# Optimization experiments

Measured on AMD Instinct MI355X. Metric: run time of the kernel, lower is better.

## Reference

```python
import jax, jax.numpy as jnp
import numpy as np

EPS = 1e-12          # matches torch F.normalize eps
NOW = 3600.0         # fixed 'current time'; timestamps are in [0,1)
TIME_DECAY = 3600.0  # temporal decay constant from the module

def setup_inputs() -> dict:
    key = jax.random.key(0)
    k1, k2, k3, k4, k5 = jax.random.split(key, 5)
    M, D, S = 100000, 768, 2
    return {
        "query_features": jax.random.normal(k1, (D,), dtype=jnp.float32),
        "location": jax.random.normal(k2, (S,), dtype=jnp.float32),
        "memory_features": jax.random.normal(k3, (M, D), dtype=jnp.float32),
        "memory_locations": jax.random.normal(k4, (M, S), dtype=jnp.float32),
        "memory_metadata": jax.random.uniform(k5, (M, 4), dtype=jnp.float32),
        "k": 5,
    }

def reference(query_features, location, memory_features, memory_locations, memory_metadata, k):
    # --- cosine similarity: normalize query and memory rows (F.normalize semantics) ---
    q_norm = query_features / jnp.maximum(jnp.linalg.norm(query_features), EPS)      # [D]
    m_norms = jnp.maximum(jnp.linalg.norm(memory_features, axis=1, keepdims=True), EPS)
    m_norm = memory_features / m_norms                                               # [M, D]
    sim_scores = m_norm @ q_norm                                                     # [M] GEMV

    # --- spatial score: 1 / (1 + euclidean distance to query location) ---
    dists = jnp.linalg.norm(memory_locations - location[None, :], axis=1)            # [M]
    spatial_scores = 1.0 / (1.0 + dists)

    # --- temporal score: exp(-age / 3600) ---
    strengths = memory_metadata[:, 0]
    timestamps = memory_metadata[:, 1]
    ages = NOW - timestamps
    temporal_scores = jnp.exp(-ages / TIME_DECAY)

    combined = (0.5 * sim_scores + 0.3 * spatial_scores + 0.2 * temporal_scores) * strengths

    top_scores, top_indices = jax.lax.top_k(combined, k)
    return top_scores, top_indices
```

## Files before the change

kernel.cpp:

```cpp
#include <hip/hip_runtime.h>
#include <math.h>

#define EPS   1e-12f
#define NOW_T 3600.0f
#define TDEC  3600.0f
#define K     5
#define D     768

__global__ __launch_bounds__(256) void score_kernel(
    const float* __restrict__ q,
    const float* __restrict__ loc,
    const float* __restrict__ feat,
    const float* __restrict__ mloc,
    const float* __restrict__ meta,
    float* __restrict__ scores,
    int M)
{
    const int tid = threadIdx.x;
    const int c   = tid & 15;
    const int g   = tid >> 4;
    const int row = blockIdx.x * 16 + g;

    const float* qp = q + c * 4;
    float4 qv[12];
    float qss = 0.f;
    #pragma unroll
    for (int j = 0; j < 12; ++j) {
        qv[j] = *(const float4*)(qp + j * 64);
        qss = fmaf(qv[j].x, qv[j].x, qss);
        qss = fmaf(qv[j].y, qv[j].y, qss);
        qss = fmaf(qv[j].z, qv[j].z, qss);
        qss = fmaf(qv[j].w, qv[j].w, qss);
    }
    #pragma unroll
    for (int m = 1; m < 16; m <<= 1) qss += __shfl_xor(qss, m);
    const float inv_qn = 1.0f / fmaxf(sqrtf(qss), EPS);

    float dot = 0.f, ss = 0.f;
    if (row < M) {
        const float* r = feat + (size_t)row * D + c * 4;
        #pragma unroll
        for (int j = 0; j < 12; ++j) {
            float4 f = *(const float4*)(r + j * 64);
            dot = fmaf(f.x, qv[j].x, dot); ss = fmaf(f.x, f.x, ss);
            dot = fmaf(f.y, qv[j].y, dot); ss = fmaf(f.y, f.y, ss);
            dot = fmaf(f.z, qv[j].z, dot); ss = fmaf(f.z, f.z, ss);
            dot = fmaf(f.w, qv[j].w, dot); ss = fmaf(f.w, f.w, ss);
        }
    }
    #pragma unroll
    for (int m = 1; m < 16; m <<= 1) {
        dot += __shfl_xor(dot, m);
        ss  += __shfl_xor(ss,  m);
    }

    if (row < M && c == 0) {
        float sim = dot * inv_qn / fmaxf(sqrtf(ss), EPS);
        float2 ml = *(const float2*)(mloc + (size_t)row * 2);
        float4 md = *(const float4*)(meta + (size_t)row * 4);
        float dx = ml.x - loc[0], dy = ml.y - loc[1];
        float dist = sqrtf(dx * dx + dy * dy);
        float spatial  = 1.0f / (1.0f + dist);
        float temporal = expf((md.y - NOW_T) / TDEC);
        scores[row] = (0.5f * sim + 0.3f * spatial + 0.2f * temporal) * md.x;
    }
}

__device__ __forceinline__ void consider(float (&v)[K], int (&ix)[K], float s, int i)
{
    if (s > v[K - 1]) {
        int j = K - 1;
        #pragma unroll
        for (int t = K - 1; t > 0; --t) {
            if (v[t - 1] < s) { v[t] = v[t - 1]; ix[t] = ix[t - 1]; j = t - 1; }
        }
        v[j] = s; ix[j] = i;
    }
}

__global__ __launch_bounds__(1024) void topk_kernel(
    const float* __restrict__ scores, int M, float* __restrict__ out)
{
    __shared__ float s_val[1024 * K];
    __shared__ int   s_idx[1024 * K];

    const int tid = threadIdx.x;
    float v[K]; int ix[K];
    #pragma unroll
    for (int j = 0; j < K; ++j) { v[j] = -INFINITY; ix[j] = -1; }

    const int M4 = M >> 2;
    const float4* s4 = (const float4*)scores;
    for (int i = tid; i < M4; i += 1024) {
        float4 s = s4[i];
        consider(v, ix, s.x, 4 * i + 0);
        consider(v, ix, s.y, 4 * i + 1);
        consider(v, ix, s.z, 4 * i + 2);
        consider(v, ix, s.w, 4 * i + 3);
    }
    for (int i = (M4 << 2) + tid; i < M; i += 1024)
        consider(v, ix, scores[i], i);

    #pragma unroll
    for (int j = 0; j < K; ++j) { s_val[tid * K + j] = v[j]; s_idx[tid * K + j] = ix[j]; }
    __syncthreads();

    for (int sz = 1024 >> 1; sz >= 1; sz >>= 1) {
        if (tid < sz) {
            const float* pv = &s_val[(tid + sz) * K];
            const int*   pi = &s_idx[(tid + sz) * K];
            float mv[K]; int mi[K];
            int a = 0, b = 0;
            #pragma unroll
            for (int j = 0; j < K; ++j) {
                bool takeA = (b >= K) || (a < K && v[a] >= pv[b]);
                if (takeA) { mv[j] = v[a];  mi[j] = ix[a]; ++a; }
                else       { mv[j] = pv[b]; mi[j] = pi[b]; ++b; }
            }
            #pragma unroll
            for (int j = 0; j < K; ++j) {
                v[j] = mv[j]; ix[j] = mi[j];
                s_val[tid * K + j] = v[j]; s_idx[tid * K + j] = ix[j];
            }
        }
        __syncthreads();
    }

    if (tid == 0) {
        #pragma unroll
        for (int j = 0; j < K; ++j) {
            out[j]     = v[j];
            out[K + j] = (float)ix[j];
        }
    }
}

extern "C" void kernel_launch(void* const* d_in, const int* in_sizes, int n_in,
                              void* d_out, int out_size, void* d_ws, size_t ws_size,
                              hipStream_t stream) {
    const float* q    = (const float*)d_in[0];
    const float* loc  = (const float*)d_in[1];
    const float* feat = (const float*)d_in[2];
    const float* mloc = (const float*)d_in[3];
    const float* meta = (const float*)d_in[4];
    const int M = in_sizes[2] / D;

    float* scores = (float*)d_ws;

    score_kernel<<<(M + 15) / 16, 256, 0, stream>>>(q, loc, feat, mloc, meta, scores, M);
    topk_kernel<<<1, 1024, 0, stream>>>(scores, M, (float*)d_out);
}
```

Baseline: 448.5 us.

## Fuse scoring with per-block top-k and merge small candidate set

The scoring kernel becomes a persistent grid-stride kernel with a fixed grid of 2048 blocks. Each 16-lane group keeps a running top-5 and the block reduces these to 5 candidates written to the workspace. The single-block top-k kernel now merges only about 10K candidates instead of scanning all 100K scores, which removes the serial full-array pass and the score write and read. In exchange, each block does a serial top-k merge in thread 0, and the fixed grid size may change how the feature-matrix stream is spread across CUs.

```diff
diff --git a/kernel.cpp b/kernel.cpp
--- a/kernel.cpp
+++ b/kernel.cpp
@@ -6,20 +6,33 @@
 #define TDEC  3600.0f
 #define K     5
 #define D     768
+#define GRID  2048
 
-__global__ __launch_bounds__(256) void score_kernel(
+__device__ __forceinline__ void consider(float (&v)[K], int (&ix)[K], float s, int i)
+{
+    if (s > v[K - 1]) {
+        int j = K - 1;
+        #pragma unroll
+        for (int t = K - 1; t > 0; --t) {
+            if (v[t - 1] < s) { v[t] = v[t - 1]; ix[t] = ix[t - 1]; j = t - 1; }
+        }
+        v[j] = s; ix[j] = i;
+    }
+}
+
+__global__ __launch_bounds__(256) void score_topk_kernel(
     const float* __restrict__ q,
     const float* __restrict__ loc,
     const float* __restrict__ feat,
     const float* __restrict__ mloc,
     const float* __restrict__ meta,
-    float* __restrict__ scores,
+    float* __restrict__ cand_val,
+    int*   __restrict__ cand_idx,
     int M)
 {
     const int tid = threadIdx.x;
     const int c   = tid & 15;
     const int g   = tid >> 4;
-    const int row = blockIdx.x * 16 + g;
 
     const float* qp = q + c * 4;
     float4 qv[12];
@@ -36,50 +49,68 @@
     for (int m = 1; m < 16; m <<= 1) qss += __shfl_xor(qss, m);
     const float inv_qn = 1.0f / fmaxf(sqrtf(qss), EPS);
 
-    float dot = 0.f, ss = 0.f;
-    if (row < M) {
-        const float* r = feat + (size_t)row * D + c * 4;
+    const float lx = loc[0];
+    const float ly = loc[1];
+
+    float v[K]; int ix[K];
+    #pragma unroll
+    for (int j = 0; j < K; ++j) { v[j] = -INFINITY; ix[j] = -1; }
+
+    for (int base = blockIdx.x * 16; base < M; base += GRID * 16) {
+        const int row = base + g;
+        float dot = 0.f, ss = 0.f;
+        if (row < M) {
+            const float* r = feat + (size_t)row * D + c * 4;
+            #pragma unroll
+            for (int j = 0; j < 12; ++j) {
+                float4 f = *(const float4*)(r + j * 64);
+                dot = fmaf(f.x, qv[j].x, dot); ss = fmaf(f.x, f.x, ss);
+                dot = fmaf(f.y, qv[j].y, dot); ss = fmaf(f.y, f.y, ss);
+                dot = fmaf(f.z, qv[j].z, dot); ss = fmaf(f.z, f.z, ss);
+                dot = fmaf(f.w, qv[j].w, dot); ss = fmaf(f.w, f.w, ss);
+            }
+        }
         #pragma unroll
-        for (int j = 0; j < 12; ++j) {
-            float4 f = *(const float4*)(r + j * 64);
-            dot = fmaf(f.x, qv[j].x, dot); ss = fmaf(f.x, f.x, ss);
-            dot = fmaf(f.y, qv[j].y, dot); ss = fmaf(f.y, f.y, ss);
-            dot = fmaf(f.z, qv[j].z, dot); ss = fmaf(f.z, f.z, ss);
-            dot = fmaf(f.w, qv[j].w, dot); ss = fmaf(f.w, f.w, ss);
+        for (int m = 1; m < 16; m <<= 1) {
+            dot += __shfl_xor(dot, m);
+            ss  += __shfl_xor(ss,  m);
+        }
+        if (row < M && c == 0) {
+            float sim = dot * inv_qn / fmaxf(sqrtf(ss), EPS);
+            float2 ml = *(const float2*)(mloc + (size_t)row * 2);
+            float4 md = *(const float4*)(meta + (size_t)row * 4);
+            float dx = ml.x - lx, dy = ml.y - ly;
+            float dist = sqrtf(dx * dx + dy * dy);
+            float spatial  = 1.0f / (1.0f + dist);
+            float temporal = expf((md.y - NOW_T) / TDEC);
+            float s = (0.5f * sim + 0.3f * spatial + 0.2f * temporal) * md.x;
+            consider(v, ix, s, row);
         }
     }
-    #pragma unroll
-    for (int m = 1; m < 16; m <<= 1) {
-        dot += __shfl_xor(dot, m);
-        ss  += __shfl_xor(ss,  m);
+
+    __shared__ float sv[16 * K];
+    __shared__ int   si[16 * K];
+    if (c == 0) {
+        #pragma unroll
+        for (int j = 0; j < K; ++j) { sv[g * K + j] = v[j]; si[g * K + j] = ix[j]; }
     }
-
-    if (row < M && c == 0) {
-        float sim = dot * inv_qn / fmaxf(sqrtf(ss), EPS);
-        float2 ml = *(const float2*)(mloc + (size_t)row * 2);
-        float4 md = *(const float4*)(meta + (size_t)row * 4);
-        float dx = ml.x - loc[0], dy = ml.y - loc[1];
-        float dist = sqrtf(dx * dx + dy * dy);
-        float spatial  = 1.0f / (1.0f + dist);
-        float temporal = expf((md.y - NOW_T) / TDEC);
-        scores[row] = (0.5f * sim + 0.3f * spatial + 0.2f * temporal) * md.x;
+    __syncthreads();
+    if (tid == 0) {
+        float bv[K]; int bi[K];
+        #pragma unroll
+        for (int j = 0; j < K; ++j) { bv[j] = -INFINITY; bi[j] = -1; }
+        for (int t = 0; t < 16 * K; ++t) consider(bv, bi, sv[t], si[t]);
+        #pragma unroll
+        for (int j = 0; j < K; ++j) {
+            cand_val[blockIdx.x * K + j] = bv[j];
+            cand_idx[blockIdx.x * K + j] = bi[j];
+        }
     }
 }
 
-__device__ __forceinline__ void consider(float (&v)[K], int (&ix)[K], float s, int i)
-{
-    if (s > v[K - 1]) {
-        int j = K - 1;
-        #pragma unroll
-        for (int t = K - 1; t > 0; --t) {
-            if (v[t - 1] < s) { v[t] = v[t - 1]; ix[t] = ix[t - 1]; j = t - 1; }
-        }
-        v[j] = s; ix[j] = i;
-    }
-}
-
-__global__ __launch_bounds__(1024) void topk_kernel(
-    const float* __restrict__ scores, int M, float* __restrict__ out)
+__global__ __launch_bounds__(1024) void merge_kernel(
+    const float* __restrict__ cand_val, const int* __restrict__ cand_idx,
+    int N, float* __restrict__ out)
 {
     __shared__ float s_val[1024 * K];
     __shared__ int   s_idx[1024 * K];
@@ -89,17 +120,8 @@
     #pragma unroll
     for (int j = 0; j < K; ++j) { v[j] = -INFINITY; ix[j] = -1; }
 
-    const int M4 = M >> 2;
-    const float4* s4 = (const float4*)scores;
-    for (int i = tid; i < M4; i += 1024) {
-        float4 s = s4[i];
-        consider(v, ix, s.x, 4 * i + 0);
-        consider(v, ix, s.y, 4 * i + 1);
-        consider(v, ix, s.z, 4 * i + 2);
-        consider(v, ix, s.w, 4 * i + 3);
-    }
-    for (int i = (M4 << 2) + tid; i < M; i += 1024)
-        consider(v, ix, scores[i], i);
+    for (int i = tid; i < N; i += 1024)
+        consider(v, ix, cand_val[i], cand_idx[i]);
 
     #pragma unroll
     for (int j = 0; j < K; ++j) { s_val[tid * K + j] = v[j]; s_idx[tid * K + j] = ix[j]; }
@@ -145,8 +167,10 @@
     const float* meta = (const float*)d_in[4];
     const int M = in_sizes[2] / D;
 
-    float* scores = (float*)d_ws;
+    float* cand_val = (float*)d_ws;
+    int*   cand_idx = (int*)((char*)d_ws + GRID * K * sizeof(float));
 
-    score_kernel<<<(M + 15) / 16, 256, 0, stream>>>(q, loc, feat, mloc, meta, scores, M);
-    topk_kernel<<<1, 1024, 0, stream>>>(scores, M, (float*)d_out);
+    score_topk_kernel<<<GRID, 256, 0, stream>>>(q, loc, feat, mloc, meta,
+                                                cand_val, cand_idx, M);
+    merge_kernel<<<1, 1024, 0, stream>>>(cand_val, cand_idx, GRID * K, (float*)d_out);
 }
```

Result: faster. 434.3 us, median of 2 (-3.2%).
